# Performance work log

Measured on AMD Instinct MI355X. Metric: run time of the kernel, lower is better.

Reference implementation:

```python
import jax, jax.numpy as jnp
import numpy as np

M, K, N = 32768, 2048, 2048  # tokens, in_features, out_features
QMIN, QMAX = -128, 127


def setup_inputs() -> dict:
    key = jax.random.key(0)
    ks = jax.random.split(key, 7)
    x = jax.random.normal(ks[0], (M, K), dtype=jnp.float32).astype(jnp.float16)
    int_weight = jax.random.randint(ks[1], (N, K), QMIN, QMAX + 1, dtype=jnp.int32).astype(jnp.int8)
    # calibrated-looking asymmetric activation quant params (fp16 buffers, [num_steps]=1)
    act_delta = (jax.random.uniform(ks[2], (1,), dtype=jnp.float32) * 0.02 + 0.005).astype(jnp.float16)
    act_zp = jnp.round(jax.random.normal(ks[3], (1,), dtype=jnp.float32) * 8.0).astype(jnp.float16)
    # per-output-channel weight scales; fuse precomputed dequant buffers consistently
    w_delta = jax.random.uniform(ks[4], (N,), dtype=jnp.float32) * 0.002 + 1e-4
    act_times_weight_delta = (act_delta.astype(jnp.float32) * w_delta)[None, :]  # [1, N]
    w_row_sum = jnp.sum(int_weight.astype(jnp.float32), axis=1)  # [N]
    zp_times_weight_channel_sum = (act_zp.astype(jnp.float32) * w_row_sum * act_times_weight_delta[0])[None, :]  # [1, N]
    bias = jax.random.normal(ks[5], (N,), dtype=jnp.float32) * 0.02
    return {
        "input": x,
        "act_delta": act_delta,
        "act_zp": act_zp,
        "zp_times_weight_channel_sum": zp_times_weight_channel_sum,
        "act_times_weight_delta": act_times_weight_delta,
        "bias": bias,
        "int_weight": int_weight,
    }


def reference(input, act_delta, act_zp, zp_times_weight_channel_sum,
              act_times_weight_delta, bias, int_weight):
    # current_step == num_steps - 1 == 0
    delta = act_delta[0].astype(jnp.float32)
    zp = act_zp[0].astype(jnp.float32)
    atwd = act_times_weight_delta[0]            # [N] = act_delta * weight_delta
    zp_sum = zp_times_weight_channel_sum[0]     # [N] = zp * rowsum(W_int) * atwd
    # asymmetric int8 activation quantization: q = clip(round(x/delta + zp))
    q = jnp.clip(jnp.round(input.astype(jnp.float32) / delta + zp), QMIN, QMAX).astype(jnp.int8)
    # int8 GEMM with int32 accumulation: [M,K] x [K,N]
    acc = jnp.matmul(q.astype(jnp.int32), int_weight.astype(jnp.int32).T)
    # fused dequant + zero-point correction + bias, cast to fp16
    out = acc.astype(jnp.float32) * atwd - zp_sum + bias
    return out.astype(jnp.float16)
```

## Files before the change

kernel.cpp:

```cpp
#include <hip/hip_runtime.h>
#include <hip/hip_fp16.h>
#include <stdint.h>

typedef int i32x4 __attribute__((ext_vector_type(4)));

#define BM 256
#define BN 256
#define BKB 64
#define NSLOT 4
#define SLOT_BYTES 32768
#define THREADS 512

__device__ __forceinline__ void gload_lds16(const void* g, void* l) {
  __builtin_amdgcn_global_load_lds(
      (const __attribute__((address_space(1))) unsigned int*)g,
      (__attribute__((address_space(3))) unsigned int*)l, 16, 0, 0);
}

__global__ __launch_bounds__(256) void quant_x_kernel(
    const float* __restrict__ x, const float* __restrict__ deltap,
    const float* __restrict__ zpp, int8_t* __restrict__ q, int n16) {
  const float rdelta = 1.0f / deltap[0];
  const float zp = zpp[0];
  for (int i = blockIdx.x * blockDim.x + threadIdx.x; i < n16;
       i += gridDim.x * blockDim.x) {
    const float4* src = (const float4*)x + (size_t)i * 4;
    int packed[4];
#pragma unroll
    for (int g = 0; g < 4; ++g) {
      float4 v = src[g];
      float f0 = fminf(127.f, fmaxf(-128.f, rintf(fmaf(v.x, rdelta, zp))));
      float f1 = fminf(127.f, fmaxf(-128.f, rintf(fmaf(v.y, rdelta, zp))));
      float f2 = fminf(127.f, fmaxf(-128.f, rintf(fmaf(v.z, rdelta, zp))));
      float f3 = fminf(127.f, fmaxf(-128.f, rintf(fmaf(v.w, rdelta, zp))));
      int q0 = (int)f0 & 255, q1 = (int)f1 & 255, q2 = (int)f2 & 255, q3 = (int)f3 & 255;
      packed[g] = q0 | (q1 << 8) | (q2 << 16) | (q3 << 24);
    }
    ((int4*)q)[i] = make_int4(packed[0], packed[1], packed[2], packed[3]);
  }
}

__global__ __launch_bounds__(256) void pack_w_kernel(
    const int* __restrict__ w, int8_t* __restrict__ wp, int n16) {
  int i = blockIdx.x * blockDim.x + threadIdx.x;
  if (i >= n16) return;
  const int4* src = (const int4*)w + (size_t)i * 4;
  int packed[4];
#pragma unroll
  for (int g = 0; g < 4; ++g) {
    int4 v = src[g];
    packed[g] = (v.x & 255) | ((v.y & 255) << 8) | ((v.z & 255) << 16) | ((v.w & 255) << 24);
  }
  ((int4*)wp)[i] = make_int4(packed[0], packed[1], packed[2], packed[3]);
}

__global__ __launch_bounds__(THREADS, 2) void gemm_i8_kernel(
    const int8_t* __restrict__ Aq, const int8_t* __restrict__ Bw,
    const float* __restrict__ atwd, const float* __restrict__ zpws,
    const float* __restrict__ bias, float* __restrict__ out,
    int Mc, int Nc, int Kc) {
  __shared__ int8_t lds[NSLOT * SLOT_BYTES];

  const int nwg = gridDim.x;
  int bid = blockIdx.x;
  if ((nwg & 7) == 0) bid = (bid & 7) * (nwg >> 3) + (bid >> 3);
  const int nbn = Nc / BN;
  const int bm = bid / nbn;
  const int bn = bid % nbn;

  const int tid = threadIdx.x;
  const size_t K = (size_t)Kc;
  const int NT = Kc / BKB;

  const int srow = tid >> 2;
  const int lc = (tid & 3) ^ ((tid >> 3) & 3);
  const int8_t* gA = Aq + ((size_t)(bm * BM + srow)) * K + lc * 16;
  const int8_t* gB = Bw + ((size_t)(bn * BN + srow)) * K + lc * 16;
  const size_t half_off = (size_t)128 * K;
  int8_t* ldst = &lds[tid * 16];

  auto stageA = [&](int t) {
    int8_t* l = ldst + (t & 3) * SLOT_BYTES;
    gload_lds16(gA + (size_t)t * BKB, l);
    gload_lds16(gA + (size_t)t * BKB + half_off, l + 8192);
  };
  auto stageB = [&](int t) {
    int8_t* l = ldst + (t & 3) * SLOT_BYTES + 16384;
    gload_lds16(gB + (size_t)t * BKB, l);
    gload_lds16(gB + (size_t)t * BKB + half_off, l + 8192);
  };

  const int lane = tid & 63;
  const int wave = tid >> 6;
  const int wr = wave >> 2;
  const int wc = wave & 3;
  const int fr = lane & 15;
  const int kc = lane >> 4;
  const int coff = ((kc ^ ((fr >> 1) & 3)) << 4);
  const int aRow = wr * 128 + fr;
  const int bRow = wc * 64 + fr;

  i32x4 acc[8][4] = {};

  stageA(0); stageB(0);
  if (NT > 1) { stageA(1); stageB(1); }
  if (NT > 2) { stageA(2); stageB(2); }
  if (NT > 2)      asm volatile("s_waitcnt vmcnt(8)" ::: "memory");
  else if (NT > 1) asm volatile("s_waitcnt vmcnt(4)" ::: "memory");
  else             asm volatile("s_waitcnt vmcnt(0)" ::: "memory");
  __builtin_amdgcn_s_barrier();
  __builtin_amdgcn_sched_barrier(0);

  for (int t = 0; t < NT; ++t) {
    const int8_t* sA = &lds[(t & 3) * SLOT_BYTES];
    const int8_t* sB = sA + 16384;

    i32x4 bfr[4], a0[4], a1[4];
#pragma unroll
    for (int j = 0; j < 4; ++j)
      bfr[j] = *(const i32x4*)&sB[(bRow + j * 16) * 64 + coff];
#pragma unroll
    for (int i = 0; i < 4; ++i)
      a0[i] = *(const i32x4*)&sA[(aRow + i * 16) * 64 + coff];
#pragma unroll
    for (int i = 0; i < 4; ++i)
      a1[i] = *(const i32x4*)&sA[(aRow + 64 + i * 16) * 64 + coff];

    if (t + 3 < NT) { stageA(t + 3); stageB(t + 3); }

#pragma unroll
    for (int i = 0; i < 4; ++i)
#pragma unroll
      for (int j = 0; j < 4; ++j)
        acc[i][j] = __builtin_amdgcn_mfma_i32_16x16x64_i8(a0[i], bfr[j], acc[i][j], 0, 0, 0);
#pragma unroll
    for (int i = 0; i < 4; ++i)
#pragma unroll
      for (int j = 0; j < 4; ++j)
        acc[4 + i][j] = __builtin_amdgcn_mfma_i32_16x16x64_i8(a1[i], bfr[j], acc[4 + i][j], 0, 0, 0);

    if (t < NT - 1) {
      if (t + 3 < NT)       asm volatile("s_waitcnt vmcnt(8)" ::: "memory");
      else if (t + 3 == NT) asm volatile("s_waitcnt vmcnt(4)" ::: "memory");
      else                  asm volatile("s_waitcnt vmcnt(0)" ::: "memory");
      __builtin_amdgcn_s_barrier();
      __builtin_amdgcn_sched_barrier(0);
    }
  }

  const int r4 = (lane >> 4) << 2;
  const int cn0 = bn * BN + wc * 64 + fr;
  float aw4[4], zs4[4], bs4[4];
#pragma unroll
  for (int j = 0; j < 4; ++j) {
    aw4[j] = atwd[cn0 + j * 16];
    zs4[j] = zpws[cn0 + j * 16];
    bs4[j] = bias[cn0 + j * 16];
  }
#pragma unroll
  for (int mi = 0; mi < 8; ++mi) {
#pragma unroll
    for (int r = 0; r < 4; ++r) {
      const size_t rbase = (size_t)(bm * BM + wr * 128 + mi * 16 + r4 + r) * (size_t)Nc;
#pragma unroll
      for (int j = 0; j < 4; ++j) {
        float v = (float)acc[mi][j][r] * aw4[j] - zs4[j] + bs4[j];
        v = __half2float(__float2half(v));
        out[rbase + cn0 + j * 16] = v;
      }
    }
  }
}

extern "C" void kernel_launch(void* const* d_in, const int* in_sizes, int n_in,
                              void* d_out, int out_size, void* d_ws, size_t ws_size,
                              hipStream_t stream) {
  const float* x         = (const float*)d_in[0];
  const float* act_delta = (const float*)d_in[1];
  const float* act_zp    = (const float*)d_in[2];
  const float* zpws      = (const float*)d_in[3];
  const float* atwd      = (const float*)d_in[4];
  const float* bias      = (const float*)d_in[5];
  const int*   w32       = (const int*)d_in[6];
  float* out = (float*)d_out;

  const int N = in_sizes[5];
  const int K = in_sizes[6] / N;
  const int M = in_sizes[0] / K;

  int8_t* q  = (int8_t*)d_ws;
  int8_t* wp = q + (size_t)M * K;

  {
    int n16 = (M * K) / 16;
    int grid = (n16 + 255) / 256;
    if (grid > 2048) grid = 2048;
    quant_x_kernel<<<grid, 256, 0, stream>>>(x, act_delta, act_zp, q, n16);
  }
  {
    int n16 = (N * K) / 16;
    pack_w_kernel<<<(n16 + 255) / 256, 256, 0, stream>>>(w32, wp, n16);
  }
  {
    dim3 grid((M / BM) * (N / BN));
    gemm_i8_kernel<<<grid, THREADS, 0, stream>>>(q, wp, atwd, zpws, bias, out, M, N, K);
  }
}
```

Baseline: 252.5 us.

## Shrink GEMM tile to 128x256 with 3-slot pipeline for higher occupancy

Halves the M tile from 256 to 128 and drops from a 4-slot prefetch-3 LDS ring to a 3-slot prefetch-2 ring, cutting LDS per block from 128KB to 72KB. Accumulators shrink from 8x4 to 4x4 per wave. Launch bounds now ask for 4 blocks per CU, meant to raise occupancy and latency hiding. The cost is lower arithmetic intensity per LDS byte: each B fragment is reused half as often and B tiles are loaded twice as often globally. The shallower prefetch also gives less time to hide load latency within each block.

Result: faster. 247.4 us (-2.0%).

```diff
diff --git a/kernel.cpp b/kernel.cpp
--- a/kernel.cpp
+++ b/kernel.cpp
@@ -4,11 +4,11 @@
 
 typedef int i32x4 __attribute__((ext_vector_type(4)));
 
-#define BM 256
+#define BM 128
 #define BN 256
 #define BKB 64
-#define NSLOT 4
-#define SLOT_BYTES 32768
+#define NSLOT 3
+#define SLOT_BYTES 24576
 #define THREADS 512
 
 __device__ __forceinline__ void gload_lds16(const void* g, void* l) {
@@ -54,7 +54,7 @@
   ((int4*)wp)[i] = make_int4(packed[0], packed[1], packed[2], packed[3]);
 }
 
-__global__ __launch_bounds__(THREADS, 2) void gemm_i8_kernel(
+__global__ __launch_bounds__(THREADS, 4) void gemm_i8_kernel(
     const int8_t* __restrict__ Aq, const int8_t* __restrict__ Bw,
     const float* __restrict__ atwd, const float* __restrict__ zpws,
     const float* __restrict__ bias, float* __restrict__ out,
@@ -76,18 +76,15 @@
   const int lc = (tid & 3) ^ ((tid >> 3) & 3);
   const int8_t* gA = Aq + ((size_t)(bm * BM + srow)) * K + lc * 16;
   const int8_t* gB = Bw + ((size_t)(bn * BN + srow)) * K + lc * 16;
-  const size_t half_off = (size_t)128 * K;
+  const size_t bHalf = (size_t)128 * K;
   int8_t* ldst = &lds[tid * 16];
 
-  auto stageA = [&](int t) {
-    int8_t* l = ldst + (t & 3) * SLOT_BYTES;
-    gload_lds16(gA + (size_t)t * BKB, l);
-    gload_lds16(gA + (size_t)t * BKB + half_off, l + 8192);
-  };
-  auto stageB = [&](int t) {
-    int8_t* l = ldst + (t & 3) * SLOT_BYTES + 16384;
-    gload_lds16(gB + (size_t)t * BKB, l);
-    gload_lds16(gB + (size_t)t * BKB + half_off, l + 8192);
+  auto stage = [&](int t, int slot) {
+    int8_t* l = ldst + slot * SLOT_BYTES;
+    const size_t koff = (size_t)t * BKB;
+    gload_lds16(gA + koff, l);
+    gload_lds16(gB + koff, l + 8192);
+    gload_lds16(gB + koff + bHalf, l + 16384);
   };
 
   const int lane = tid & 63;
@@ -97,55 +94,49 @@
   const int fr = lane & 15;
   const int kc = lane >> 4;
   const int coff = ((kc ^ ((fr >> 1) & 3)) << 4);
-  const int aRow = wr * 128 + fr;
+  const int aRow = wr * 64 + fr;
   const int bRow = wc * 64 + fr;
 
-  i32x4 acc[8][4] = {};
+  i32x4 acc[4][4] = {};
 
-  stageA(0); stageB(0);
-  if (NT > 1) { stageA(1); stageB(1); }
-  if (NT > 2) { stageA(2); stageB(2); }
-  if (NT > 2)      asm volatile("s_waitcnt vmcnt(8)" ::: "memory");
-  else if (NT > 1) asm volatile("s_waitcnt vmcnt(4)" ::: "memory");
-  else             asm volatile("s_waitcnt vmcnt(0)" ::: "memory");
+  stage(0, 0);
+  if (NT > 1) stage(1, 1);
+  if (NT > 1) asm volatile("s_waitcnt vmcnt(3)" ::: "memory");
+  else        asm volatile("s_waitcnt vmcnt(0)" ::: "memory");
   __builtin_amdgcn_s_barrier();
   __builtin_amdgcn_sched_barrier(0);
 
+  int rs = 0;
   for (int t = 0; t < NT; ++t) {
-    const int8_t* sA = &lds[(t & 3) * SLOT_BYTES];
-    const int8_t* sB = sA + 16384;
+    const int8_t* sA = &lds[rs * SLOT_BYTES];
+    const int8_t* sB = sA + 8192;
 
-    i32x4 bfr[4], a0[4], a1[4];
+    i32x4 afr[4], bfr[4];
 #pragma unroll
     for (int j = 0; j < 4; ++j)
       bfr[j] = *(const i32x4*)&sB[(bRow + j * 16) * 64 + coff];
 #pragma unroll
     for (int i = 0; i < 4; ++i)
-      a0[i] = *(const i32x4*)&sA[(aRow + i * 16) * 64 + coff];
-#pragma unroll
-    for (int i = 0; i < 4; ++i)
-      a1[i] = *(const i32x4*)&sA[(aRow + 64 + i * 16) * 64 + coff];
+      afr[i] = *(const i32x4*)&sA[(aRow + i * 16) * 64 + coff];
 
-    if (t + 3 < NT) { stageA(t + 3); stageB(t + 3); }
+    if (t + 2 < NT) {
+      int ws = rs + 2; if (ws >= NSLOT) ws -= NSLOT;
+      stage(t + 2, ws);
+    }
 
 #pragma unroll
     for (int i = 0; i < 4; ++i)
 #pragma unroll
       for (int j = 0; j < 4; ++j)
-        acc[i][j] = __builtin_amdgcn_mfma_i32_16x16x64_i8(a0[i], bfr[j], acc[i][j], 0, 0, 0);
-#pragma unroll
-    for (int i = 0; i < 4; ++i)
-#pragma unroll
-      for (int j = 0; j < 4; ++j)
-        acc[4 + i][j] = __builtin_amdgcn_mfma_i32_16x16x64_i8(a1[i], bfr[j], acc[4 + i][j], 0, 0, 0);
+        acc[i][j] = __builtin_amdgcn_mfma_i32_16x16x64_i8(afr[i], bfr[j], acc[i][j], 0, 0, 0);
 
     if (t < NT - 1) {
-      if (t + 3 < NT)       asm volatile("s_waitcnt vmcnt(8)" ::: "memory");
-      else if (t + 3 == NT) asm volatile("s_waitcnt vmcnt(4)" ::: "memory");
-      else                  asm volatile("s_waitcnt vmcnt(0)" ::: "memory");
+      if (t + 2 < NT) asm volatile("s_waitcnt vmcnt(3)" ::: "memory");
+      else            asm volatile("s_waitcnt vmcnt(0)" ::: "memory");
       __builtin_amdgcn_s_barrier();
       __builtin_amdgcn_sched_barrier(0);
     }
+    rs = rs + 1; if (rs >= NSLOT) rs -= NSLOT;
   }
 
   const int r4 = (lane >> 4) << 2;
@@ -158,10 +149,10 @@
     bs4[j] = bias[cn0 + j * 16];
   }
 #pragma unroll
-  for (int mi = 0; mi < 8; ++mi) {
+  for (int mi = 0; mi < 4; ++mi) {
 #pragma unroll
     for (int r = 0; r < 4; ++r) {
-      const size_t rbase = (size_t)(bm * BM + wr * 128 + mi * 16 + r4 + r) * (size_t)Nc;
+      const size_t rbase = (size_t)(bm * BM + wr * 64 + mi * 16 + r4 + r) * (size_t)Nc;
 #pragma unroll
       for (int j = 0; j < 4; ++j) {
         float v = (float)acc[mi][j][r] * aw4[j] - zs4[j] + bs4[j];
```

## Replace workgroup barriers with per-slot LDS flag polling between waves

Applied to the files above, without the earlier changes.

Replaces the per-iteration s_barrier in the int8 GEMM main loop with per-slot arrival and consumption byte flags in LDS. Each wave publishes its flag bytes with atomic stores and spins until all 8 waves match. Waves can then drift apart instead of lockstepping, and MFMA sections are raised with s_setprio. The spin-polling costs LDS traffic and issue slots, and correctness depends on the ordering between the global_load_lds writes and the flag stores.

Measured after the change: 273.3 us. 1.08x slower.

```diff
diff --git a/kernel.cpp b/kernel.cpp
--- a/kernel.cpp
+++ b/kernel.cpp
@@ -15,6 +15,15 @@
   __builtin_amdgcn_global_load_lds(
       (const __attribute__((address_space(1))) unsigned int*)g,
       (__attribute__((address_space(3))) unsigned int*)l, 16, 0, 0);
+}
+
+__device__ __forceinline__ void poll_eq(unsigned long long* f,
+                                        unsigned long long expect) {
+  while (__atomic_load_n(f, __ATOMIC_RELAXED) != expect) { }
+  __builtin_amdgcn_sched_barrier(0);
+}
+__device__ __forceinline__ unsigned long long splat8(int id) {
+  return 0x0101010101010101ull * (unsigned long long)(id & 255);
 }
 
 __global__ __launch_bounds__(256) void quant_x_kernel(
@@ -60,6 +69,8 @@
     const float* __restrict__ bias, float* __restrict__ out,
     int Mc, int Nc, int Kc) {
   __shared__ int8_t lds[NSLOT * SLOT_BYTES];
+  __shared__ unsigned long long g_arr[NSLOT];
+  __shared__ unsigned long long g_con[NSLOT];
 
   const int nwg = gridDim.x;
   int bid = blockIdx.x;
@@ -72,6 +83,12 @@
   const size_t K = (size_t)Kc;
   const int NT = Kc / BKB;
 
+  if (tid == 0) {
+#pragma unroll
+    for (int s = 0; s < NSLOT; ++s) { g_arr[s] = ~0ull; g_con[s] = ~0ull; }
+  }
+  __syncthreads();
+
   const int srow = tid >> 2;
   const int lc = (tid & 3) ^ ((tid >> 3) & 3);
   const int8_t* gA = Aq + ((size_t)(bm * BM + srow)) * K + lc * 16;
@@ -79,15 +96,13 @@
   const size_t half_off = (size_t)128 * K;
   int8_t* ldst = &lds[tid * 16];
 
-  auto stageA = [&](int t) {
+  auto stage = [&](int t) {
     int8_t* l = ldst + (t & 3) * SLOT_BYTES;
-    gload_lds16(gA + (size_t)t * BKB, l);
-    gload_lds16(gA + (size_t)t * BKB + half_off, l + 8192);
-  };
-  auto stageB = [&](int t) {
-    int8_t* l = ldst + (t & 3) * SLOT_BYTES + 16384;
-    gload_lds16(gB + (size_t)t * BKB, l);
-    gload_lds16(gB + (size_t)t * BKB + half_off, l + 8192);
+    const size_t koff = (size_t)t * BKB;
+    gload_lds16(gA + koff, l);
+    gload_lds16(gA + koff + half_off, l + 8192);
+    gload_lds16(gB + koff, l + 16384);
+    gload_lds16(gB + koff + half_off, l + 24576);
   };
 
   const int lane = tid & 63;
@@ -102,19 +117,33 @@
 
   i32x4 acc[8][4] = {};
 
-  stageA(0); stageB(0);
-  if (NT > 1) { stageA(1); stageB(1); }
-  if (NT > 2) { stageA(2); stageB(2); }
-  if (NT > 2)      asm volatile("s_waitcnt vmcnt(8)" ::: "memory");
-  else if (NT > 1) asm volatile("s_waitcnt vmcnt(4)" ::: "memory");
-  else             asm volatile("s_waitcnt vmcnt(0)" ::: "memory");
-  __builtin_amdgcn_s_barrier();
-  __builtin_amdgcn_sched_barrier(0);
+  stage(0); stage(1); stage(2);
+  asm volatile("s_waitcnt vmcnt(8)" ::: "memory");
+  if (lane == 0)
+    __atomic_store_n((unsigned char*)&g_arr[0] + wave, (unsigned char)0,
+                     __ATOMIC_RELAXED);
 
   for (int t = 0; t < NT; ++t) {
-    const int8_t* sA = &lds[(t & 3) * SLOT_BYTES];
+    const int s = t & 3;
+
+    if (t + 3 < NT) {
+      if (t + 3 >= NSLOT) poll_eq(&g_con[(t + 3) & 3], splat8(t - 1));
+      stage(t + 3);
+    }
+    if (t + 1 < NT) {
+      const int last = (t + 3 < NT) ? (t + 3) : (NT - 1);
+      const int cnt = last - t;
+      if (cnt >= 3)      asm volatile("s_waitcnt vmcnt(8)" ::: "memory");
+      else if (cnt == 2) asm volatile("s_waitcnt vmcnt(4)" ::: "memory");
+      else               asm volatile("s_waitcnt vmcnt(0)" ::: "memory");
+      if (lane == 0)
+        __atomic_store_n((unsigned char*)&g_arr[(t + 1) & 3] + wave,
+                         (unsigned char)((t + 1) & 255), __ATOMIC_RELAXED);
+    }
+    poll_eq(&g_arr[s], splat8(t));
+
+    const int8_t* sA = &lds[s * SLOT_BYTES];
     const int8_t* sB = sA + 16384;
-
     i32x4 bfr[4], a0[4], a1[4];
 #pragma unroll
     for (int j = 0; j < 4; ++j)
@@ -125,9 +154,12 @@
 #pragma unroll
     for (int i = 0; i < 4; ++i)
       a1[i] = *(const i32x4*)&sA[(aRow + 64 + i * 16) * 64 + coff];
-
-    if (t + 3 < NT) { stageA(t + 3); stageB(t + 3); }
-
+    asm volatile("s_waitcnt lgkmcnt(0)" ::: "memory");
+    __builtin_amdgcn_sched_barrier(0);
+    if (lane == 0)
+      __atomic_store_n((unsigned char*)&g_con[s] + wave,
+                       (unsigned char)(t & 255), __ATOMIC_RELAXED);
+    __builtin_amdgcn_s_setprio(1);
 #pragma unroll
     for (int i = 0; i < 4; ++i)
 #pragma unroll
@@ -138,14 +170,7 @@
 #pragma unroll
       for (int j = 0; j < 4; ++j)
         acc[4 + i][j] = __builtin_amdgcn_mfma_i32_16x16x64_i8(a1[i], bfr[j], acc[4 + i][j], 0, 0, 0);
-
-    if (t < NT - 1) {
-      if (t + 3 < NT)       asm volatile("s_waitcnt vmcnt(8)" ::: "memory");
-      else if (t + 3 == NT) asm volatile("s_waitcnt vmcnt(4)" ::: "memory");
-      else                  asm volatile("s_waitcnt vmcnt(0)" ::: "memory");
-      __builtin_amdgcn_s_barrier();
-      __builtin_amdgcn_sched_barrier(0);
-    }
+    __builtin_amdgcn_s_setprio(0);
   }
 
   const int r4 = (lane >> 4) << 2;
```
